# Kernel optimization log

Measured on AMD Instinct MI355X. Metric: run time of the kernel, lower is better.

## Reference

```python
import jax, jax.numpy as jnp
import numpy as np

EPS = 1e-12  # torch F.normalize eps

def _l2norm(t):
    # normalize over last axis (N), clamp norm like torch.nn.functional.normalize
    n = jnp.linalg.norm(t, axis=-1, keepdims=True)
    return t / jnp.maximum(n, EPS)

def setup_inputs() -> dict:
    key = jax.random.key(0)
    ks = jax.random.split(key, 4)
    B, N, D, H = 8, 4096, 768, 16
    x = jax.random.normal(ks[0], (B, N, D), dtype=jnp.float32)
    w_qkv = jax.random.normal(ks[1], (D, 3 * D), dtype=jnp.float32) * (D ** -0.5)
    temperature = jnp.ones((H, 1, 1), dtype=jnp.float32)
    w_proj = jax.random.normal(ks[2], (D, D), dtype=jnp.float32) * (D ** -0.5)
    b_proj = jnp.zeros((D,), dtype=jnp.float32)
    return {"x": x, "w_qkv": w_qkv, "temperature": temperature,
            "w_proj": w_proj, "b_proj": b_proj}

def reference(x, w_qkv, temperature, w_proj, b_proj):
    B, N, D = x.shape
    H = temperature.shape[0]
    C = D // H
    # qkv linear (no bias), split last dim as (3, H, C), move to (3, B, H, C, N)
    qkv = (x @ w_qkv).reshape(B, N, 3, H, C).transpose(2, 0, 3, 4, 1)
    q, k, v = qkv[0], qkv[1], qkv[2]            # each [B, H, C, N]
    q = _l2norm(q)
    k = _l2norm(k)
    # cross-covariance attention: small CxC matrix per head
    attn = jnp.einsum('bhcn,bhdn->bhcd', q, k) * temperature  # [B,H,C,C]
    attn = jax.nn.softmax(attn, axis=-1)
    out = jnp.einsum('bhcd,bhdn->bhcn', attn, v)  # [B,H,C,N]
    out = out.transpose(0, 3, 1, 2).reshape(B, N, D)  # B N (H C)
    return out @ w_proj + b_proj
```

## Files before the change

kernel.cpp:

```cpp
#include <hip/hip_runtime.h>
#include <stdint.h>

typedef __attribute__((ext_vector_type(4))) float          f32x4;
typedef __attribute__((ext_vector_type(8))) short          bf16x8;
typedef __attribute__((ext_vector_type(8))) unsigned short u16x8;
typedef __attribute__((ext_vector_type(4))) unsigned short u16x4;

static __device__ __forceinline__ unsigned short f2bf(float f){
  uint32_t u = __builtin_bit_cast(uint32_t, f);
  u += 0x7FFFu + ((u >> 16) & 1u);
  return (unsigned short)(u >> 16);
}
static __device__ __forceinline__ float bf2f(unsigned short h){
  uint32_t u = ((uint32_t)h) << 16;
  return __builtin_bit_cast(float, u);
}

__global__ void k_cvt(const float* __restrict__ in, unsigned short* __restrict__ out, long n){
  long i = ((long)blockIdx.x * blockDim.x + threadIdx.x) * 8;
  if (i >= n) return;
  const f32x4* p = (const f32x4*)(in + i);
  f32x4 a = p[0], b = p[1];
  u16x8 o;
  #pragma unroll
  for (int j = 0; j < 4; j++){ o[j] = f2bf(a[j]); o[4+j] = f2bf(b[j]); }
  *(u16x8*)(out + i) = o;
}

__global__ void k_cvtwv(const float* __restrict__ w, unsigned short* __restrict__ out){
  const long idx = ((long)blockIdx.x * blockDim.x + threadIdx.x) * 8;
  const int e = (int)(idx / 768), hd = (int)(idx - (long)e * 768);
  const float* s = w + (long)e * 2304 + 1536 + hd;
  f32x4 a = *(const f32x4*)s, b = *(const f32x4*)(s + 4);
  u16x8 o;
  #pragma unroll
  for (int j = 0; j < 4; j++){ o[j] = f2bf(a[j]); o[4+j] = f2bf(b[j]); }
  *(u16x8*)(out + idx) = o;
}

__global__ void k_tconv(const float* __restrict__ in, unsigned short* __restrict__ out, int R, int C){
  __shared__ float tl[64][65];
  const int c0 = blockIdx.x * 64, r0 = blockIdx.y * 64;
  const int t = threadIdx.x;
  {
    const int lr = t >> 2, lc = (t & 3) * 16;
    const f32x4* s = (const f32x4*)(in + (long)(r0 + lr) * C + c0 + lc);
    #pragma unroll
    for (int q = 0; q < 4; q++){
      f32x4 v = s[q];
      #pragma unroll
      for (int j = 0; j < 4; j++) tl[lr][lc + q*4 + j] = v[j];
    }
  }
  __syncthreads();
  {
    const int oc = t >> 2, orr = (t & 3) * 16;
    u16x8 o0, o1;
    #pragma unroll
    for (int i = 0; i < 8; i++){ o0[i] = f2bf(tl[orr + i][oc]); o1[i] = f2bf(tl[orr + 8 + i][oc]); }
    u16x8* dst = (u16x8*)(out + (long)(c0 + oc) * R + r0 + orr);
    dst[0] = o0; dst[1] = o1;
  }
}


static __device__ __forceinline__ void stageA(const unsigned short* __restrict__ G, int row0, int ke,
                                              char* slot, int t){
  const int r  = t >> 2;
  const int ko = (t & 3) ^ ((r ^ (r >> 2)) & 3);
  const char* src = (const char*)(G + (long)(row0 + r) * 768 + ke + ko * 8);
  char* dst = slot + (t & 0x1C0) * 16;
  __builtin_amdgcn_global_load_lds((const __attribute__((address_space(1))) unsigned int*)src,
                                   (__attribute__((address_space(3))) unsigned int*)dst, 16, 0, 0);
}
static __device__ __forceinline__ void stageB(const unsigned short* __restrict__ G, int row0, int ke,
                                              char* slot, int t){
  #pragma unroll
  for (int l = 0; l < 2; l++){
    const int r  = l*128 + (t >> 2);
    const int ko = (t & 3) ^ ((r ^ (r >> 2)) & 3);
    const char* src = (const char*)(G + (long)(row0 + r) * 768 + ke + ko * 8);
    char* dst = slot + l*8192 + (t & 0x1C0) * 16;
    __builtin_amdgcn_global_load_lds((const __attribute__((address_space(1))) unsigned int*)src,
                                     (__attribute__((address_space(3))) unsigned int*)dst, 16, 0, 0);
  }
}

static __device__ __forceinline__ bf16x8 ldfrag(const char* slot, int row, int ko){
  const int k2 = (ko ^ (row ^ (row >> 2))) & 3;
  return *(const bf16x8*)(slot + row*64 + k2*16);
}

#define VM3 asm volatile("s_waitcnt vmcnt(3)" ::: "memory")
#define VM0 asm volatile("s_waitcnt vmcnt(0)" ::: "memory")

#define PHASE1(CUR, STAGE_STMT, WAIT_STMT) do {                                \
    bf16x8 af[4], bq[4];                                                       \
    _Pragma("unroll")                                                          \
    for (int ni = 0; ni < 4; ni++)                                             \
      bq[ni] = ldfrag(sB[CUR], wn*64 + ni*16 + arow, ko);                      \
    _Pragma("unroll")                                                          \
    for (int mi = 0; mi < 4; mi++)                                             \
      af[mi] = ldfrag(sA[CUR], wm*64 + mi*16 + arow, ko);                      \
    __builtin_amdgcn_s_barrier();                                              \
    __builtin_amdgcn_s_setprio(1);                                             \
    _Pragma("unroll")                                                          \
    for (int mi = 0; mi < 4; mi++)                                             \
      _Pragma("unroll")                                                        \
      for (int ni = 0; ni < 4; ni++)                                           \
        acc[mi][ni] = __builtin_amdgcn_mfma_f32_16x16x32_bf16(                 \
            af[mi], bq[ni], acc[mi][ni], 0, 0, 0);                             \
    __builtin_amdgcn_s_setprio(0);                                             \
    STAGE_STMT;                                                                \
    WAIT_STMT;                                                                 \
    __builtin_amdgcn_s_barrier();                                              \
  } while(0)

template<int MODE>
__global__ __launch_bounds__(512, 4)
void k_gemm3(const unsigned short* __restrict__ A, const unsigned short* __restrict__ BT,
             unsigned short* __restrict__ QT, unsigned short* __restrict__ KT,
             float* __restrict__ OUTF, const float* __restrict__ bias,
             float* __restrict__ nrmp)
{
  __shared__ __attribute__((aligned(16))) char lds[73728];
  constexpr int NT = (MODE == 0) ? 6 : 3;
  constexpr int NWG = 256 * NT;
  const int o  = blockIdx.x;
  const int wg = (o & 7) * (NWG >> 3) + (o >> 3);
  const int jt = wg % NT, mt = wg / NT;
  const int m0 = mt * 128, j0 = jt * 256;
  const int t = threadIdx.x, lane = t & 63, w = t >> 6;
  const int wm = w >> 2, wn = w & 3;
  const int arow = lane & 15, ko = lane >> 4;
  const unsigned short* BTb = (MODE == 1) ? BT + ((long)(m0 >> 12)) * 768 * 768 : BT;

  char* const sA[3] = {lds,          lds + 8192,          lds + 16384};
  char* const sB[3] = {lds + 24576,  lds + 24576 + 16384, lds + 24576 + 32768};

  f32x4 acc[4][4] = {};

  stageA(A, m0, 0,  sA[0], t);  stageB(BTb, j0, 0,  sB[0], t);
  stageA(A, m0, 32, sA[1], t);  stageB(BTb, j0, 32, sB[1], t);
  VM3;
  __builtin_amdgcn_s_barrier();

  #pragma unroll 1
  for (int g = 0; g < 7; ++g){
    const int ke2 = g * 96;
    PHASE1(0, { stageA(A, m0, ke2+64,  sA[2], t); stageB(BTb, j0, ke2+64,  sB[2], t); }, VM3);
    PHASE1(1, { stageA(A, m0, ke2+96,  sA[0], t); stageB(BTb, j0, ke2+96,  sB[0], t); }, VM3);
    PHASE1(2, { stageA(A, m0, ke2+128, sA[1], t); stageB(BTb, j0, ke2+128, sB[1], t); }, VM3);
  }
  PHASE1(0, { stageA(A, m0, 736, sA[2], t); stageB(BTb, j0, 736, sB[2], t); }, VM3);
  PHASE1(1, { ; }, VM0);
  PHASE1(2, { ; }, ;);

  if (MODE == 0){
    const int b = m0 >> 12;
    const int nb = (m0 & 4095) + wm*64 + (lane >> 4)*4;
    #pragma unroll
    for (int mi = 0; mi < 4; mi++){
      #pragma unroll
      for (int ni = 0; ni < 4; ni++){
        const int jc = j0 + wn*64 + ni*16 + (lane & 15);
        const int s  = (jc >= 768);
        const int jl = jc - s * 768;
        const int h  = jl / 48;
        const int c  = jl - h * 48;
        unsigned short* dst = (s ? KT : QT) + (((long)(b*16 + h) * 48 + c) << 12) + nb + mi*16;
        u16x4 pk;
        #pragma unroll
        for (int r = 0; r < 4; r++) pk[r] = f2bf(acc[mi][ni][r]);
        *(u16x4*)dst = pk;
      }
    }
    const int chunk = ((m0 & 4095) >> 6) + wm;
    #pragma unroll
    for (int ni = 0; ni < 4; ni++){
      float ss = 0.f;
      #pragma unroll
      for (int mi = 0; mi < 4; mi++)
        #pragma unroll
        for (int r = 0; r < 4; r++) ss += acc[mi][ni][r] * acc[mi][ni][r];
      ss += __shfl_xor(ss, 16);
      ss += __shfl_xor(ss, 32);
      if (lane < 16){
        const int jc = j0 + wn*64 + ni*16 + lane;
        const int s  = (jc >= 768);
        const int jl = jc - s * 768;
        const int h  = jl / 48;
        const int c  = jl - h * 48;
        const int prow = s*6144 + (b*16 + h)*48 + c;
        nrmp[(long)prow*64 + chunk] = ss;
      }
    }
  } else {
    #pragma unroll
    for (int mi = 0; mi < 4; mi++){
      #pragma unroll
      for (int ni = 0; ni < 4; ni++){
        const int jc = j0 + wn*64 + ni*16 + (lane & 15);
        const float bv = bias[jc];
        const long mr = (long)m0 + wm*64 + mi*16 + (lane >> 4)*4;
        #pragma unroll
        for (int r = 0; r < 4; r++) OUTF[(mr + r) * 768 + jc] = acc[mi][ni][r] + bv;
      }
    }
  }
}

__global__ __launch_bounds__(256)
void k_attn_part(const unsigned short* __restrict__ QT, const unsigned short* __restrict__ KT,
                 float* __restrict__ Spart)
{
  __shared__ float Sl[4][2304];
  const int bh = blockIdx.x, ksp = blockIdx.y;
  const int t = threadIdx.x, lane = t & 63, w = t >> 6;
  const unsigned short* qb = QT + ((long)bh * 48 << 12);
  const unsigned short* kb = KT + ((long)bh * 48 << 12);
  const int n00 = ksp * 1024 + w * 256;
  f32x4 acc[3][3] = {};
  for (int kt = 0; kt < 256; kt += 32){
    bf16x8 af[3], bfr[3];
    #pragma unroll
    for (int ci = 0; ci < 3; ci++)
      af[ci]  = *(const bf16x8*)(qb + ((long)(ci*16 + (lane & 15)) << 12) + n00 + kt + (lane >> 4) * 8);
    #pragma unroll
    for (int di = 0; di < 3; di++)
      bfr[di] = *(const bf16x8*)(kb + ((long)(di*16 + (lane & 15)) << 12) + n00 + kt + (lane >> 4) * 8);
    #pragma unroll
    for (int ci = 0; ci < 3; ci++)
      #pragma unroll
      for (int di = 0; di < 3; di++)
        acc[ci][di] = __builtin_amdgcn_mfma_f32_16x16x32_bf16(af[ci], bfr[di], acc[ci][di], 0, 0, 0);
  }
  #pragma unroll
  for (int ci = 0; ci < 3; ci++)
    #pragma unroll
    for (int di = 0; di < 3; di++)
      #pragma unroll
      for (int r = 0; r < 4; r++)
        Sl[w][(ci*16 + (lane >> 4)*4 + r) * 48 + di*16 + (lane & 15)] = acc[ci][di][r];
  __syncthreads();
  float* outp = Spart + ((long)ksp * 128 + bh) * 2304;
  for (int idx = t; idx < 2304; idx += 256)
    outp[idx] = Sl[0][idx] + Sl[1][idx] + Sl[2][idx] + Sl[3][idx];
}

__global__ void k_softmax(const float* __restrict__ Spart, const float* __restrict__ nrmp,
                          const float* __restrict__ temp, unsigned short* __restrict__ attnT)
{
  __shared__ float invq[48], invk[48];
  const int bh = blockIdx.x, h = bh & 15;
  const int c = threadIdx.x;
  if (c < 48){
    float sq = 0.f, sk = 0.f;
    const float* pq = nrmp + (long)(bh*48 + c) * 64;
    const float* pk = nrmp + (long)(6144 + bh*48 + c) * 64;
    #pragma unroll
    for (int i = 0; i < 64; i++){ sq += pq[i]; sk += pk[i]; }
    invq[c] = 1.0f / fmaxf(sqrtf(sq), 1e-12f);
    invk[c] = 1.0f / fmaxf(sqrtf(sk), 1e-12f);
  }
  __syncthreads();
  if (c < 48){
    const float scq = invq[c] * temp[h];
    float row[48];
    #pragma unroll
    for (int d = 0; d < 48; d++){
      long base = ((long)bh * 48 + c) * 48 + d;
      float v = Spart[base] + Spart[base + 128L*2304] + Spart[base + 256L*2304] + Spart[base + 384L*2304];
      row[d] = v * scq * invk[d];
    }
    float mx = -1e30f;
    #pragma unroll
    for (int d = 0; d < 48; d++) mx = fmaxf(mx, row[d]);
    float s = 0.f;
    #pragma unroll
    for (int d = 0; d < 48; d++){ row[d] = expf(row[d] - mx); s += row[d]; }
    const float inv = 1.0f / s;
    unsigned short* ob = attnT + (long)bh * 48 * 64;
    #pragma unroll
    for (int d = 0; d < 48; d++) ob[d*64 + c] = f2bf(row[d] * inv);
    u16x8 z = {};
    *(u16x8*)(ob + c*64 + 48) = z;
    *(u16x8*)(ob + c*64 + 56) = z;
  }
}

__global__ __launch_bounds__(256)
void k_wmod2(const unsigned short* __restrict__ WpT, const unsigned short* __restrict__ attnT,
             unsigned short* __restrict__ WmodT)
{
  const int j0 = blockIdx.x * 256, h = blockIdx.y, b = blockIdx.z;
  const int t = threadIdx.x, lane = t & 63, w = t >> 6;
  const unsigned short* wp = WpT + h * 48;
  const unsigned short* ab = attnT + ((long)(b*16 + h)) * 48 * 64;
  f32x4 acc[4][3] = {};
  #pragma unroll
  for (int kt = 0; kt < 64; kt += 32){
    bf16x8 bfr[3];
    #pragma unroll
    for (int ni = 0; ni < 3; ni++)
      bfr[ni] = *(const bf16x8*)(ab + (ni*16 + (lane & 15))*64 + kt + (lane >> 4)*8);
    #pragma unroll
    for (int mi = 0; mi < 4; mi++){
      const int j = j0 + w*64 + mi*16 + (lane & 15);
      bf16x8 a = *(const bf16x8*)(wp + (long)j*768 + kt + (lane >> 4)*8);
      #pragma unroll
      for (int ni = 0; ni < 3; ni++)
        acc[mi][ni] = __builtin_amdgcn_mfma_f32_16x16x32_bf16(a, bfr[ni], acc[mi][ni], 0, 0, 0);
    }
  }
  #pragma unroll
  for (int mi = 0; mi < 4; mi++)
    #pragma unroll
    for (int ni = 0; ni < 3; ni++)
      #pragma unroll
      for (int r = 0; r < 4; r++){
        const int j = j0 + w*64 + mi*16 + (lane >> 4)*4 + r;
        const int d = ni*16 + (lane & 15);
        WmodT[(long)b*589824 + (long)j*768 + h*48 + d] = f2bf(acc[mi][ni][r]);
      }
}

__global__ __launch_bounds__(256)
void k_comb(const unsigned short* __restrict__ A, const unsigned short* __restrict__ BT,
            unsigned short* __restrict__ OUT)
{
  __shared__ unsigned short As[128 * 32];
  __shared__ unsigned short Bs[128 * 32];
  const int m0 = blockIdx.y * 128;
  const int j0 = blockIdx.x * 128;
  const int t = threadIdx.x;
  const int lane = t & 63;
  const int w = t >> 6, wm = w >> 1, wn = w & 1;

  f32x4 acc[4][4] = {};

  for (int kt = 0; kt < 768; kt += 32){
    if (kt) __syncthreads();
    #pragma unroll
    for (int i = 0; i < 2; i++){
      const char* ga = (const char*)A  + (long)(m0 + i*64 + (t >> 2)) * 1536 + kt*2 + (t & 3) * 16;
      const char* gb = (const char*)BT + (long)(j0 + i*64 + (t >> 2)) * 1536 + kt*2 + (t & 3) * 16;
      char* la = (char*)As + i*4096 + (t & 0xC0) * 16;
      char* lb = (char*)Bs + i*4096 + (t & 0xC0) * 16;
      __builtin_amdgcn_global_load_lds((const __attribute__((address_space(1))) unsigned int*)ga,
                                       (__attribute__((address_space(3))) unsigned int*)la, 16, 0, 0);
      __builtin_amdgcn_global_load_lds((const __attribute__((address_space(1))) unsigned int*)gb,
                                       (__attribute__((address_space(3))) unsigned int*)lb, 16, 0, 0);
    }
    __syncthreads();
    bf16x8 af[4], bfr[4];
    #pragma unroll
    for (int mi = 0; mi < 4; mi++)
      af[mi]  = *(const bf16x8*)&As[(wm*64 + mi*16 + (lane & 15)) * 32 + (lane >> 4) * 8];
    #pragma unroll
    for (int ni = 0; ni < 4; ni++)
      bfr[ni] = *(const bf16x8*)&Bs[(wn*64 + ni*16 + (lane & 15)) * 32 + (lane >> 4) * 8];
    #pragma unroll
    for (int mi = 0; mi < 4; mi++)
      #pragma unroll
      for (int ni = 0; ni < 4; ni++)
        acc[mi][ni] = __builtin_amdgcn_mfma_f32_16x16x32_bf16(af[mi], bfr[ni], acc[mi][ni], 0, 0, 0);
  }

  #pragma unroll
  for (int mi = 0; mi < 4; mi++)
    #pragma unroll
    for (int ni = 0; ni < 4; ni++){
      const int jc = j0 + wn*64 + ni*16 + (lane & 15);
      const long mr = (long)m0 + wm*64 + mi*16 + (lane >> 4) * 4;
      #pragma unroll
      for (int r = 0; r < 4; r++) OUT[(mr + r) * 768 + jc] = f2bf(acc[mi][ni][r]);
    }
}

extern "C" void kernel_launch(void* const* d_in, const int* in_sizes, int n_in,
                              void* d_out, int out_size, void* d_ws, size_t ws_size,
                              hipStream_t stream)
{
  (void)in_sizes; (void)n_in; (void)out_size; (void)ws_size;
  const float* x      = (const float*)d_in[0];
  const float* w_qkv  = (const float*)d_in[1];
  const float* temp   = (const float*)d_in[2];
  const float* w_proj = (const float*)d_in[3];
  const float* b_proj = (const float*)d_in[4];
  float* outF = (float*)d_out;

  char* ws = (char*)d_ws;
  size_t off = 0;
  auto alloc = [&](size_t bytes)->char*{ char* p = ws + off; off += (bytes + 255) & ~(size_t)255; return p; };

  unsigned short* x_bf  = (unsigned short*)alloc(50331648);
  unsigned short* WT    = (unsigned short*)alloc(3538944);
  unsigned short* WpT   = (unsigned short*)alloc(1179648);
  unsigned short* WvB   = (unsigned short*)alloc(1179648);
  unsigned short* QT    = (unsigned short*)alloc(100663296);
  unsigned short* KT    = QT + (long)6144 * 4096;
  float* nrmp           = (float*)alloc(12288L * 64 * 4);
  float* Spart          = (float*)alloc(4L * 128 * 2304 * 4);
  unsigned short* attnT = (unsigned short*)alloc(128L * 48 * 64 * 2);
  unsigned short* WmodT = (unsigned short*)alloc(9437184);
  unsigned short* WcombT= (unsigned short*)alloc(9437184);

  k_cvt<<<12288, 256, 0, stream>>>(x, x_bf, 25165824L);
  k_tconv<<<dim3(36, 12), 256, 0, stream>>>(w_qkv, WT, 768, 2304);
  k_tconv<<<dim3(12, 12), 256, 0, stream>>>(w_proj, WpT, 768, 768);
  k_cvtwv<<<288, 256, 0, stream>>>(w_qkv, WvB);
  k_gemm3<0><<<1536, 512, 0, stream>>>(x_bf, WT, QT, KT, nullptr, nullptr, nrmp);
  k_attn_part<<<dim3(128, 4), 256, 0, stream>>>(QT, KT, Spart);
  k_softmax<<<128, 64, 0, stream>>>(Spart, nrmp, temp, attnT);
  k_wmod2<<<dim3(3, 16, 8), 256, 0, stream>>>(WpT, attnT, WmodT);
  k_comb<<<dim3(6, 48), 256, 0, stream>>>(WmodT, WvB, WcombT);
  k_gemm3<1><<<768, 512, 0, stream>>>(x_bf, WcombT, nullptr, nullptr, outF, b_proj, nullptr);
}
```

Before: 253.2 us.

## Load GEMM B operand directly to registers, shrink LDS to A-only ring

The B-tile (weight) fragments are now loaded straight from global memory into registers per wave, one K-step ahead, instead of being staged through LDS. This shrinks LDS from 72KB to 24KB, which may raise occupancy, and removes the LDS write/read traffic for B. The A-fragment loads are split so MFMAs can start after only two A reads, and wait counts are adjusted for the new load mix. The trade-off is that each wave issues its own uncoalesced-strided global loads for B with no sharing across waves, which adds L2 traffic and exposes global latency.

```diff
diff --git a/kernel.cpp b/kernel.cpp
--- a/kernel.cpp
+++ b/kernel.cpp
@@ -73,57 +73,63 @@
   __builtin_amdgcn_global_load_lds((const __attribute__((address_space(1))) unsigned int*)src,
                                    (__attribute__((address_space(3))) unsigned int*)dst, 16, 0, 0);
 }
-static __device__ __forceinline__ void stageB(const unsigned short* __restrict__ G, int row0, int ke,
-                                              char* slot, int t){
-  #pragma unroll
-  for (int l = 0; l < 2; l++){
-    const int r  = l*128 + (t >> 2);
-    const int ko = (t & 3) ^ ((r ^ (r >> 2)) & 3);
-    const char* src = (const char*)(G + (long)(row0 + r) * 768 + ke + ko * 8);
-    char* dst = slot + l*8192 + (t & 0x1C0) * 16;
-    __builtin_amdgcn_global_load_lds((const __attribute__((address_space(1))) unsigned int*)src,
-                                     (__attribute__((address_space(3))) unsigned int*)dst, 16, 0, 0);
-  }
-}
 
 static __device__ __forceinline__ bf16x8 ldfrag(const char* slot, int row, int ko){
   const int k2 = (ko ^ (row ^ (row >> 2))) & 3;
   return *(const bf16x8*)(slot + row*64 + k2*16);
 }
 
-#define VM3 asm volatile("s_waitcnt vmcnt(3)" ::: "memory")
-#define VM0 asm volatile("s_waitcnt vmcnt(0)" ::: "memory")
-
-#define PHASE1(CUR, STAGE_STMT, WAIT_STMT) do {                                \
-    bf16x8 af[4], bq[4];                                                       \
-    _Pragma("unroll")                                                          \
-    for (int ni = 0; ni < 4; ni++)                                             \
-      bq[ni] = ldfrag(sB[CUR], wn*64 + ni*16 + arow, ko);                      \
-    _Pragma("unroll")                                                          \
-    for (int mi = 0; mi < 4; mi++)                                             \
-      af[mi] = ldfrag(sA[CUR], wm*64 + mi*16 + arow, ko);                      \
-    __builtin_amdgcn_s_barrier();                                              \
-    __builtin_amdgcn_s_setprio(1);                                             \
-    _Pragma("unroll")                                                          \
-    for (int mi = 0; mi < 4; mi++)                                             \
+#define MFMA_(a,b,c) __builtin_amdgcn_mfma_f32_16x16x32_bf16(a,b,c,0,0,0)
+
+#define LDB4(KE)                                                               \
+    bqv[0] = *(const bf16x8*)(bbase + (KE));                                   \
+    bqv[1] = *(const bf16x8*)(bbase + 12288 + (KE));                           \
+    bqv[2] = *(const bf16x8*)(bbase + 24576 + (KE));                           \
+    bqv[3] = *(const bf16x8*)(bbase + 36864 + (KE));
+
+#define POSTN(KE1, SLOT2, KE2)                                                 \
+    LDB4(KE1)                                                                  \
+    stageA(A, m0, (KE2), (SLOT2), t);                                          \
+    __builtin_amdgcn_sched_barrier(0);                                         \
+    asm volatile("s_waitcnt vmcnt(5)" ::: "memory");                           \
+    __builtin_amdgcn_s_barrier();
+
+#define POSTT                                                                  \
+    LDB4(736)                                                                  \
+    __builtin_amdgcn_sched_barrier(0);                                         \
+    asm volatile("s_waitcnt vmcnt(4)" ::: "memory");                           \
+    __builtin_amdgcn_s_barrier();
+
+#define PH(CUR, POST) do {                                                     \
+    {                                                                          \
+      bf16x8 a0 = ldfrag(sA[CUR], wm64 +  0 + arow, ko);                       \
+      bf16x8 a1 = ldfrag(sA[CUR], wm64 + 16 + arow, ko);                       \
+      __builtin_amdgcn_s_setprio(1);                                           \
       _Pragma("unroll")                                                        \
-      for (int ni = 0; ni < 4; ni++)                                           \
-        acc[mi][ni] = __builtin_amdgcn_mfma_f32_16x16x32_bf16(                 \
-            af[mi], bq[ni], acc[mi][ni], 0, 0, 0);                             \
-    __builtin_amdgcn_s_setprio(0);                                             \
-    STAGE_STMT;                                                                \
-    WAIT_STMT;                                                                 \
-    __builtin_amdgcn_s_barrier();                                              \
+      for (int ni = 0; ni < 4; ni++) acc[0][ni] = MFMA_(a0, bqv[ni], acc[0][ni]); \
+      _Pragma("unroll")                                                        \
+      for (int ni = 0; ni < 4; ni++) acc[1][ni] = MFMA_(a1, bqv[ni], acc[1][ni]); \
+    }                                                                          \
+    {                                                                          \
+      bf16x8 a2 = ldfrag(sA[CUR], wm64 + 32 + arow, ko);                       \
+      bf16x8 a3 = ldfrag(sA[CUR], wm64 + 48 + arow, ko);                       \
+      _Pragma("unroll")                                                        \
+      for (int ni = 0; ni < 4; ni++) acc[2][ni] = MFMA_(a2, bqv[ni], acc[2][ni]); \
+      _Pragma("unroll")                                                        \
+      for (int ni = 0; ni < 4; ni++) acc[3][ni] = MFMA_(a3, bqv[ni], acc[3][ni]); \
+      __builtin_amdgcn_s_setprio(0);                                           \
+    }                                                                          \
+    POST                                                                       \
   } while(0)
 
 template<int MODE>
 __global__ __launch_bounds__(512, 4)
-void k_gemm3(const unsigned short* __restrict__ A, const unsigned short* __restrict__ BT,
+void k_gemm4(const unsigned short* __restrict__ A, const unsigned short* __restrict__ BT,
              unsigned short* __restrict__ QT, unsigned short* __restrict__ KT,
              float* __restrict__ OUTF, const float* __restrict__ bias,
              float* __restrict__ nrmp)
 {
-  __shared__ __attribute__((aligned(16))) char lds[73728];
+  __shared__ __attribute__((aligned(16))) char lds[24576];
   constexpr int NT = (MODE == 0) ? 6 : 3;
   constexpr int NWG = 256 * NT;
   const int o  = blockIdx.x;
@@ -132,29 +138,33 @@
   const int m0 = mt * 128, j0 = jt * 256;
   const int t = threadIdx.x, lane = t & 63, w = t >> 6;
   const int wm = w >> 2, wn = w & 3;
+  const int wm64 = wm * 64;
   const int arow = lane & 15, ko = lane >> 4;
-  const unsigned short* BTb = (MODE == 1) ? BT + ((long)(m0 >> 12)) * 768 * 768 : BT;
-
-  char* const sA[3] = {lds,          lds + 8192,          lds + 16384};
-  char* const sB[3] = {lds + 24576,  lds + 24576 + 16384, lds + 24576 + 32768};
+  const unsigned short* BTb = (MODE == 1) ? BT + ((long)(m0 >> 12)) * 589824 : BT;
+  const unsigned short* bbase = BTb + (long)(j0 + wn*64 + arow) * 768 + ko * 8;
+
+  char* const sA[3] = {lds, lds + 8192, lds + 16384};
 
   f32x4 acc[4][4] = {};
-
-  stageA(A, m0, 0,  sA[0], t);  stageB(BTb, j0, 0,  sB[0], t);
-  stageA(A, m0, 32, sA[1], t);  stageB(BTb, j0, 32, sB[1], t);
-  VM3;
+  bf16x8 bqv[4];
+
+  stageA(A, m0, 0,  sA[0], t);
+  stageA(A, m0, 32, sA[1], t);
+  LDB4(0)
+  __builtin_amdgcn_sched_barrier(0);
+  asm volatile("s_waitcnt vmcnt(5)" ::: "memory");
   __builtin_amdgcn_s_barrier();
 
   #pragma unroll 1
   for (int g = 0; g < 7; ++g){
-    const int ke2 = g * 96;
-    PHASE1(0, { stageA(A, m0, ke2+64,  sA[2], t); stageB(BTb, j0, ke2+64,  sB[2], t); }, VM3);
-    PHASE1(1, { stageA(A, m0, ke2+96,  sA[0], t); stageB(BTb, j0, ke2+96,  sB[0], t); }, VM3);
-    PHASE1(2, { stageA(A, m0, ke2+128, sA[1], t); stageB(BTb, j0, ke2+128, sB[1], t); }, VM3);
-  }
-  PHASE1(0, { stageA(A, m0, 736, sA[2], t); stageB(BTb, j0, 736, sB[2], t); }, VM3);
-  PHASE1(1, { ; }, VM0);
-  PHASE1(2, { ; }, ;);
+    const int kb = g * 96;
+    PH(0, POSTN(kb + 32,  sA[2], kb + 64));
+    PH(1, POSTN(kb + 64,  sA[0], kb + 96));
+    PH(2, POSTN(kb + 96,  sA[1], kb + 128));
+  }
+  PH(0, POSTN(704, sA[2], 736));
+  PH(1, POSTT);
+  PH(2, {});
 
   if (MODE == 0){
     const int b = m0 >> 12;
@@ -410,10 +420,10 @@
   k_tconv<<<dim3(36, 12), 256, 0, stream>>>(w_qkv, WT, 768, 2304);
   k_tconv<<<dim3(12, 12), 256, 0, stream>>>(w_proj, WpT, 768, 768);
   k_cvtwv<<<288, 256, 0, stream>>>(w_qkv, WvB);
-  k_gemm3<0><<<1536, 512, 0, stream>>>(x_bf, WT, QT, KT, nullptr, nullptr, nrmp);
+  k_gemm4<0><<<1536, 512, 0, stream>>>(x_bf, WT, QT, KT, nullptr, nullptr, nrmp);
   k_attn_part<<<dim3(128, 4), 256, 0, stream>>>(QT, KT, Spart);
   k_softmax<<<128, 64, 0, stream>>>(Spart, nrmp, temp, attnT);
   k_wmod2<<<dim3(3, 16, 8), 256, 0, stream>>>(WpT, attnT, WmodT);
   k_comb<<<dim3(6, 48), 256, 0, stream>>>(WmodT, WvB, WcombT);
-  k_gemm3<1><<<768, 512, 0, stream>>>(x_bf, WcombT, nullptr, nullptr, outF, b_proj, nullptr);
-}
+  k_gemm4<1><<<768, 512, 0, stream>>>(x_bf, WcombT, nullptr, nullptr, outF, b_proj, nullptr);
+}
```

Measured after the change: 340.1 us. +34.3%, slower.

## Fuse QK^T cross-covariance into the QK projection GEMM epilogue

Applied to the files above, without the earlier changes.

Reorders the Q/K columns of the qkv weight so each 192-wide tile holds the Q and K channels of two heads. The QK GEMM then computes partial C×C q·k^T products from its 128-token tile in LDS, instead of writing 100MB of bf16 Q/K to global memory and reading it back in a separate kernel. Partial sums are spread over 32 token chunks, and softmax now reduces these larger partial buffers. The GEMM uses 384-thread blocks with a simpler LDS swizzle, and the extra epilogue MFMA work and partial-reduction traffic are the tradeoff.

```diff
diff --git a/kernel.cpp b/kernel.cpp
--- a/kernel.cpp
+++ b/kernel.cpp
@@ -63,22 +63,58 @@
   }
 }
 
-
-static __device__ __forceinline__ void stageA(const unsigned short* __restrict__ G, int row0, int ke,
-                                              char* slot, int t){
+static __device__ __forceinline__ int mapW(int j){
+  const int isK = (j >= 768);
+  const int jj = j - isK * 768;
+  const int h = jj / 48, c = jj - h * 48;
+  return (h >> 1) * 192 + (h & 1) * 96 + isK * 48 + c;
+}
+__global__ void k_tconvQK(const float* __restrict__ in, unsigned short* __restrict__ out){
+  __shared__ float tl[64][65];
+  const int c0 = blockIdx.x * 64, r0 = blockIdx.y * 64;
+  const int t = threadIdx.x;
+  {
+    const int lr = t >> 2, lc = (t & 3) * 16;
+    const f32x4* s = (const f32x4*)(in + (long)(r0 + lr) * 2304 + c0 + lc);
+    #pragma unroll
+    for (int q = 0; q < 4; q++){
+      f32x4 v = s[q];
+      #pragma unroll
+      for (int j = 0; j < 4; j++) tl[lr][lc + q*4 + j] = v[j];
+    }
+  }
+  __syncthreads();
+  {
+    const int oc = t >> 2, orr = (t & 3) * 16;
+    u16x8 o0, o1;
+    #pragma unroll
+    for (int i = 0; i < 8; i++){ o0[i] = f2bf(tl[orr + i][oc]); o1[i] = f2bf(tl[orr + 8 + i][oc]); }
+    u16x8* dst = (u16x8*)(out + (long)mapW(c0 + oc) * 768 + r0 + orr);
+    dst[0] = o0; dst[1] = o1;
+  }
+}
+
+
+static __device__ __forceinline__ bf16x8 ldfrag(const char* slot, int row, int ko){
+  const int k2 = (ko ^ (row >> 1)) & 3;
+  return *(const bf16x8*)(slot + row*64 + k2*16);
+}
+
+static __device__ __forceinline__ void stageA512(const unsigned short* __restrict__ G, int row0, int ke,
+                                                 char* slot, int t){
   const int r  = t >> 2;
-  const int ko = (t & 3) ^ ((r ^ (r >> 2)) & 3);
+  const int ko = (t & 3) ^ ((r >> 1) & 3);
   const char* src = (const char*)(G + (long)(row0 + r) * 768 + ke + ko * 8);
   char* dst = slot + (t & 0x1C0) * 16;
   __builtin_amdgcn_global_load_lds((const __attribute__((address_space(1))) unsigned int*)src,
                                    (__attribute__((address_space(3))) unsigned int*)dst, 16, 0, 0);
 }
-static __device__ __forceinline__ void stageB(const unsigned short* __restrict__ G, int row0, int ke,
-                                              char* slot, int t){
+static __device__ __forceinline__ void stageB512(const unsigned short* __restrict__ G, int row0, int ke,
+                                                 char* slot, int t){
   #pragma unroll
   for (int l = 0; l < 2; l++){
     const int r  = l*128 + (t >> 2);
-    const int ko = (t & 3) ^ ((r ^ (r >> 2)) & 3);
+    const int ko = (t & 3) ^ ((r >> 1) & 3);
     const char* src = (const char*)(G + (long)(row0 + r) * 768 + ke + ko * 8);
     char* dst = slot + l*8192 + (t & 0x1C0) * 16;
     __builtin_amdgcn_global_load_lds((const __attribute__((address_space(1))) unsigned int*)src,
@@ -86,13 +122,42 @@
   }
 }
 
-static __device__ __forceinline__ bf16x8 ldfrag(const char* slot, int row, int ko){
-  const int k2 = (ko ^ (row ^ (row >> 2))) & 3;
-  return *(const bf16x8*)(slot + row*64 + k2*16);
-}
-
+static __device__ __forceinline__ void stageA384(const unsigned short* __restrict__ G, int row0, int ke,
+                                                 char* slot, int t){
+  {
+    const int r  = t >> 2;
+    const int ko = (t & 3) ^ ((r >> 1) & 3);
+    const char* src = (const char*)(G + (long)(row0 + r) * 768 + ke + ko * 8);
+    char* dst = slot + (t & 0x1C0) * 16;
+    __builtin_amdgcn_global_load_lds((const __attribute__((address_space(1))) unsigned int*)src,
+                                     (__attribute__((address_space(3))) unsigned int*)dst, 16, 0, 0);
+  }
+  if (t < 128){
+    const int r  = 96 + (t >> 2);
+    const int ko = (t & 3) ^ ((r >> 1) & 3);
+    const char* src = (const char*)(G + (long)(row0 + r) * 768 + ke + ko * 8);
+    char* dst = slot + 6144 + (t & 0x1C0) * 16;
+    __builtin_amdgcn_global_load_lds((const __attribute__((address_space(1))) unsigned int*)src,
+                                     (__attribute__((address_space(3))) unsigned int*)dst, 16, 0, 0);
+  }
+}
+static __device__ __forceinline__ void stageB384(const unsigned short* __restrict__ G, int row0, int ke,
+                                                 char* slot, int t){
+  #pragma unroll
+  for (int l = 0; l < 2; l++){
+    const int r  = l*96 + (t >> 2);
+    const int ko = (t & 3) ^ ((r >> 1) & 3);
+    const char* src = (const char*)(G + (long)(row0 + r) * 768 + ke + ko * 8);
+    char* dst = slot + l*6144 + (t & 0x1C0) * 16;
+    __builtin_amdgcn_global_load_lds((const __attribute__((address_space(1))) unsigned int*)src,
+                                     (__attribute__((address_space(3))) unsigned int*)dst, 16, 0, 0);
+  }
+}
+
+#define VM0 asm volatile("s_waitcnt vmcnt(0)" ::: "memory")
 #define VM3 asm volatile("s_waitcnt vmcnt(3)" ::: "memory")
-#define VM0 asm volatile("s_waitcnt vmcnt(0)" ::: "memory")
+#define GATEQK { if (w < 2) asm volatile("s_waitcnt vmcnt(4)" ::: "memory");   \
+                 else       asm volatile("s_waitcnt vmcnt(3)" ::: "memory"); }
 
 #define PHASE1(CUR, STAGE_STMT, WAIT_STMT) do {                                \
     bf16x8 af[4], bq[4];                                                       \
@@ -101,7 +166,7 @@
       bq[ni] = ldfrag(sB[CUR], wn*64 + ni*16 + arow, ko);                      \
     _Pragma("unroll")                                                          \
     for (int mi = 0; mi < 4; mi++)                                             \
-      af[mi] = ldfrag(sA[CUR], wm*64 + mi*16 + arow, ko);                      \
+      af[mi] = ldfrag(sA[CUR], wm64 + mi*16 + arow, ko);                       \
     __builtin_amdgcn_s_barrier();                                              \
     __builtin_amdgcn_s_setprio(1);                                             \
     _Pragma("unroll")                                                          \
@@ -116,163 +181,187 @@
     __builtin_amdgcn_s_barrier();                                              \
   } while(0)
 
-template<int MODE>
+__global__ __launch_bounds__(384, 3)
+void k_gemmQK(const unsigned short* __restrict__ A, const unsigned short* __restrict__ BT,
+              float* __restrict__ Spart, float* __restrict__ nrmp)
+{
+  __shared__ __attribute__((aligned(16))) char lds[61440];
+  const int o  = blockIdx.x;
+  const int wg = (o & 7) * 256 + (o >> 3);
+  const int jt = wg & 7, mt = wg >> 3;
+  const int m0 = mt * 128, j0 = jt * 192;
+  const int t = threadIdx.x, lane = t & 63, w = t >> 6;
+  const int wm = w >> 2 & 1;
+  const int wmr = (w < 3) ? 0 : 1;
+  const int wn  = (w < 3) ? w : w - 3;
+  const int wm64 = wmr * 64;
+  const int arow = lane & 15, ko = lane >> 4;
+  (void)wm;
+
+  char* const sA[3] = {lds,          lds + 8192,          lds + 16384};
+  char* const sB[3] = {lds + 24576,  lds + 24576 + 12288, lds + 24576 + 24576};
+
+  f32x4 acc[4][4] = {};
+
+  stageA384(A, m0, 0,  sA[0], t);  stageB384(BT, j0, 0,  sB[0], t);
+  stageA384(A, m0, 32, sA[1], t);  stageB384(BT, j0, 32, sB[1], t);
+  GATEQK;
+  __builtin_amdgcn_s_barrier();
+
+  #pragma unroll 1
+  for (int g = 0; g < 7; ++g){
+    const int kb = g * 96;
+    PHASE1(0, { stageA384(A, m0, kb+64,  sA[2], t); stageB384(BT, j0, kb+64,  sB[2], t); }, GATEQK);
+    PHASE1(1, { stageA384(A, m0, kb+96,  sA[0], t); stageB384(BT, j0, kb+96,  sB[0], t); }, GATEQK);
+    PHASE1(2, { stageA384(A, m0, kb+128, sA[1], t); stageB384(BT, j0, kb+128, sB[1], t); }, GATEQK);
+  }
+  PHASE1(0, { stageA384(A, m0, 736, sA[2], t); stageB384(BT, j0, 736, sB[2], t); }, GATEQK);
+  PHASE1(1, { ; }, VM0);
+  PHASE1(2, { ; }, ;);
+
+  const int b = m0 >> 12;
+  const int chunk = ((m0 & 4095) >> 6) + wmr;
+  #pragma unroll
+  for (int ni = 0; ni < 4; ni++){
+    float ss = 0.f;
+    #pragma unroll
+    for (int mi = 0; mi < 4; mi++)
+      #pragma unroll
+      for (int r = 0; r < 4; r++) ss += acc[mi][ni][r] * acc[mi][ni][r];
+    ss += __shfl_xor(ss, 16);
+    ss += __shfl_xor(ss, 32);
+    if (lane < 16){
+      const int jr = wn*64 + ni*16 + lane;
+      const int hl = jr / 96, rem = jr - hl*96;
+      const int isK = (rem >= 48), c = rem - isK*48;
+      const int prow = isK*6144 + (b*16 + jt*2 + hl)*48 + c;
+      nrmp[(long)prow*64 + chunk] = ss;
+    }
+  }
+  __syncthreads();
+  #pragma unroll
+  for (int mi = 0; mi < 4; mi++){
+    #pragma unroll
+    for (int ni = 0; ni < 4; ni++){
+      const int j = wn*64 + ni*16 + (lane & 15);
+      const int n = wm64 + mi*16 + (lane >> 4)*4;
+      u16x4 pk;
+      #pragma unroll
+      for (int r = 0; r < 4; r++) pk[r] = f2bf(acc[mi][ni][r]);
+      *(u16x4*)(lds + (long)j*272 + n*2) = pk;
+    }
+  }
+  __syncthreads();
+  {
+    const int hl = (w < 3) ? 0 : 1;
+    const int ci = (w < 3) ? w : w - 3;
+    f32x4 accs[3] = {};
+    #pragma unroll
+    for (int kt = 0; kt < 128; kt += 32){
+      const bf16x8 aq = *(const bf16x8*)(lds + (long)(hl*96 + ci*16 + (lane & 15))*272
+                                             + (kt + (lane >> 4)*8)*2);
+      #pragma unroll
+      for (int di = 0; di < 3; di++){
+        const bf16x8 bk = *(const bf16x8*)(lds + (long)(hl*96 + 48 + di*16 + (lane & 15))*272
+                                               + (kt + (lane >> 4)*8)*2);
+        accs[di] = __builtin_amdgcn_mfma_f32_16x16x32_bf16(aq, bk, accs[di], 0, 0, 0);
+      }
+    }
+    const int ksp = (m0 & 4095) >> 7;
+    float* Sb = Spart + ((long)ksp*128 + b*16 + jt*2 + hl) * 2304;
+    #pragma unroll
+    for (int di = 0; di < 3; di++)
+      #pragma unroll
+      for (int r = 0; r < 4; r++){
+        const int c = ci*16 + (lane >> 4)*4 + r;
+        const int d = di*16 + (lane & 15);
+        Sb[c*48 + d] = accs[di][r];
+      }
+  }
+}
+
 __global__ __launch_bounds__(512, 4)
-void k_gemm3(const unsigned short* __restrict__ A, const unsigned short* __restrict__ BT,
-             unsigned short* __restrict__ QT, unsigned short* __restrict__ KT,
-             float* __restrict__ OUTF, const float* __restrict__ bias,
-             float* __restrict__ nrmp)
+void k_gemmP(const unsigned short* __restrict__ A, const unsigned short* __restrict__ BT,
+             float* __restrict__ OUTF, const float* __restrict__ bias)
 {
   __shared__ __attribute__((aligned(16))) char lds[73728];
-  constexpr int NT = (MODE == 0) ? 6 : 3;
-  constexpr int NWG = 256 * NT;
   const int o  = blockIdx.x;
-  const int wg = (o & 7) * (NWG >> 3) + (o >> 3);
-  const int jt = wg % NT, mt = wg / NT;
+  const int wg = (o & 7) * 96 + (o >> 3);
+  const int jt = wg % 3, mt = wg / 3;
   const int m0 = mt * 128, j0 = jt * 256;
   const int t = threadIdx.x, lane = t & 63, w = t >> 6;
   const int wm = w >> 2, wn = w & 3;
+  const int wm64 = wm * 64;
   const int arow = lane & 15, ko = lane >> 4;
-  const unsigned short* BTb = (MODE == 1) ? BT + ((long)(m0 >> 12)) * 768 * 768 : BT;
+  const unsigned short* BTb = BT + ((long)(m0 >> 12)) * 589824;
 
   char* const sA[3] = {lds,          lds + 8192,          lds + 16384};
   char* const sB[3] = {lds + 24576,  lds + 24576 + 16384, lds + 24576 + 32768};
 
   f32x4 acc[4][4] = {};
 
-  stageA(A, m0, 0,  sA[0], t);  stageB(BTb, j0, 0,  sB[0], t);
-  stageA(A, m0, 32, sA[1], t);  stageB(BTb, j0, 32, sB[1], t);
+  stageA512(A, m0, 0,  sA[0], t);  stageB512(BTb, j0, 0,  sB[0], t);
+  stageA512(A, m0, 32, sA[1], t);  stageB512(BTb, j0, 32, sB[1], t);
   VM3;
   __builtin_amdgcn_s_barrier();
 
   #pragma unroll 1
   for (int g = 0; g < 7; ++g){
-    const int ke2 = g * 96;
-    PHASE1(0, { stageA(A, m0, ke2+64,  sA[2], t); stageB(BTb, j0, ke2+64,  sB[2], t); }, VM3);
-    PHASE1(1, { stageA(A, m0, ke2+96,  sA[0], t); stageB(BTb, j0, ke2+96,  sB[0], t); }, VM3);
-    PHASE1(2, { stageA(A, m0, ke2+128, sA[1], t); stageB(BTb, j0, ke2+128, sB[1], t); }, VM3);
-  }
-  PHASE1(0, { stageA(A, m0, 736, sA[2], t); stageB(BTb, j0, 736, sB[2], t); }, VM3);
+    const int kb = g * 96;
+    PHASE1(0, { stageA512(A, m0, kb+64,  sA[2], t); stageB512(BTb, j0, kb+64,  sB[2], t); }, VM3);
+    PHASE1(1, { stageA512(A, m0, kb+96,  sA[0], t); stageB512(BTb, j0, kb+96,  sB[0], t); }, VM3);
+    PHASE1(2, { stageA512(A, m0, kb+128, sA[1], t); stageB512(BTb, j0, kb+128, sB[1], t); }, VM3);
+  }
+  PHASE1(0, { stageA512(A, m0, 736, sA[2], t); stageB512(BTb, j0, 736, sB[2], t); }, VM3);
   PHASE1(1, { ; }, VM0);
   PHASE1(2, { ; }, ;);
 
-  if (MODE == 0){
-    const int b = m0 >> 12;
-    const int nb = (m0 & 4095) + wm*64 + (lane >> 4)*4;
-    #pragma unroll
-    for (int mi = 0; mi < 4; mi++){
-      #pragma unroll
-      for (int ni = 0; ni < 4; ni++){
-        const int jc = j0 + wn*64 + ni*16 + (lane & 15);
-        const int s  = (jc >= 768);
-        const int jl = jc - s * 768;
-        const int h  = jl / 48;
-        const int c  = jl - h * 48;
-        unsigned short* dst = (s ? KT : QT) + (((long)(b*16 + h) * 48 + c) << 12) + nb + mi*16;
-        u16x4 pk;
-        #pragma unroll
-        for (int r = 0; r < 4; r++) pk[r] = f2bf(acc[mi][ni][r]);
-        *(u16x4*)dst = pk;
-      }
-    }
-    const int chunk = ((m0 & 4095) >> 6) + wm;
+  #pragma unroll
+  for (int mi = 0; mi < 4; mi++){
     #pragma unroll
     for (int ni = 0; ni < 4; ni++){
-      float ss = 0.f;
-      #pragma unroll
-      for (int mi = 0; mi < 4; mi++)
-        #pragma unroll
-        for (int r = 0; r < 4; r++) ss += acc[mi][ni][r] * acc[mi][ni][r];
-      ss += __shfl_xor(ss, 16);
-      ss += __shfl_xor(ss, 32);
-      if (lane < 16){
-        const int jc = j0 + wn*64 + ni*16 + lane;
-        const int s  = (jc >= 768);
-        const int jl = jc - s * 768;
-        const int h  = jl / 48;
-        const int c  = jl - h * 48;
-        const int prow = s*6144 + (b*16 + h)*48 + c;
-        nrmp[(long)prow*64 + chunk] = ss;
-      }
-    }
-  } else {
-    #pragma unroll
-    for (int mi = 0; mi < 4; mi++){
-      #pragma unroll
-      for (int ni = 0; ni < 4; ni++){
-        const int jc = j0 + wn*64 + ni*16 + (lane & 15);
-        const float bv = bias[jc];
-        const long mr = (long)m0 + wm*64 + mi*16 + (lane >> 4)*4;
-        #pragma unroll
-        for (int r = 0; r < 4; r++) OUTF[(mr + r) * 768 + jc] = acc[mi][ni][r] + bv;
-      }
-    }
-  }
-}
-
-__global__ __launch_bounds__(256)
-void k_attn_part(const unsigned short* __restrict__ QT, const unsigned short* __restrict__ KT,
-                 float* __restrict__ Spart)
-{
-  __shared__ float Sl[4][2304];
-  const int bh = blockIdx.x, ksp = blockIdx.y;
-  const int t = threadIdx.x, lane = t & 63, w = t >> 6;
-  const unsigned short* qb = QT + ((long)bh * 48 << 12);
-  const unsigned short* kb = KT + ((long)bh * 48 << 12);
-  const int n00 = ksp * 1024 + w * 256;
-  f32x4 acc[3][3] = {};
-  for (int kt = 0; kt < 256; kt += 32){
-    bf16x8 af[3], bfr[3];
-    #pragma unroll
-    for (int ci = 0; ci < 3; ci++)
-      af[ci]  = *(const bf16x8*)(qb + ((long)(ci*16 + (lane & 15)) << 12) + n00 + kt + (lane >> 4) * 8);
-    #pragma unroll
-    for (int di = 0; di < 3; di++)
-      bfr[di] = *(const bf16x8*)(kb + ((long)(di*16 + (lane & 15)) << 12) + n00 + kt + (lane >> 4) * 8);
-    #pragma unroll
-    for (int ci = 0; ci < 3; ci++)
-      #pragma unroll
-      for (int di = 0; di < 3; di++)
-        acc[ci][di] = __builtin_amdgcn_mfma_f32_16x16x32_bf16(af[ci], bfr[di], acc[ci][di], 0, 0, 0);
-  }
-  #pragma unroll
-  for (int ci = 0; ci < 3; ci++)
-    #pragma unroll
-    for (int di = 0; di < 3; di++)
-      #pragma unroll
-      for (int r = 0; r < 4; r++)
-        Sl[w][(ci*16 + (lane >> 4)*4 + r) * 48 + di*16 + (lane & 15)] = acc[ci][di][r];
-  __syncthreads();
-  float* outp = Spart + ((long)ksp * 128 + bh) * 2304;
-  for (int idx = t; idx < 2304; idx += 256)
-    outp[idx] = Sl[0][idx] + Sl[1][idx] + Sl[2][idx] + Sl[3][idx];
+      const int jc = j0 + wn*64 + ni*16 + (lane & 15);
+      const float bv = bias[jc];
+      const long mr = (long)m0 + wm64 + mi*16 + (lane >> 4)*4;
+      #pragma unroll
+      for (int r = 0; r < 4; r++) OUTF[(mr + r) * 768 + jc] = acc[mi][ni][r] + bv;
+    }
+  }
 }
 
 __global__ void k_softmax(const float* __restrict__ Spart, const float* __restrict__ nrmp,
                           const float* __restrict__ temp, unsigned short* __restrict__ attnT)
 {
+  __shared__ float Ss[2304];
   __shared__ float invq[48], invk[48];
   const int bh = blockIdx.x, h = bh & 15;
-  const int c = threadIdx.x;
-  if (c < 48){
+  const int t = threadIdx.x;
+  f32x4 a0[9];
+  #pragma unroll
+  for (int v = 0; v < 9; v++) a0[v] = f32x4{0.f,0.f,0.f,0.f};
+  for (int p = 0; p < 32; p++){
+    const f32x4* src = (const f32x4*)(Spart + ((long)p*128 + bh)*2304);
+    #pragma unroll
+    for (int v = 0; v < 9; v++) a0[v] += src[v*64 + t];
+  }
+  #pragma unroll
+  for (int v = 0; v < 9; v++) *(f32x4*)(Ss + (v*64 + t)*4) = a0[v];
+  if (t < 48){
     float sq = 0.f, sk = 0.f;
-    const float* pq = nrmp + (long)(bh*48 + c) * 64;
-    const float* pk = nrmp + (long)(6144 + bh*48 + c) * 64;
+    const float* pq = nrmp + (long)(bh*48 + t) * 64;
+    const float* pk = nrmp + (long)(6144 + bh*48 + t) * 64;
     #pragma unroll
     for (int i = 0; i < 64; i++){ sq += pq[i]; sk += pk[i]; }
-    invq[c] = 1.0f / fmaxf(sqrtf(sq), 1e-12f);
-    invk[c] = 1.0f / fmaxf(sqrtf(sk), 1e-12f);
+    invq[t] = 1.0f / fmaxf(sqrtf(sq), 1e-12f);
+    invk[t] = 1.0f / fmaxf(sqrtf(sk), 1e-12f);
   }
   __syncthreads();
-  if (c < 48){
+  if (t < 48){
+    const int c = t;
     const float scq = invq[c] * temp[h];
     float row[48];
     #pragma unroll
-    for (int d = 0; d < 48; d++){
-      long base = ((long)bh * 48 + c) * 48 + d;
-      float v = Spart[base] + Spart[base + 128L*2304] + Spart[base + 256L*2304] + Spart[base + 384L*2304];
-      row[d] = v * scq * invk[d];
-    }
+    for (int d = 0; d < 48; d++) row[d] = Ss[c*48 + d] * scq * invk[d];
     float mx = -1e30f;
     #pragma unroll
     for (int d = 0; d < 48; d++) mx = fmaxf(mx, row[d]);
@@ -395,25 +484,22 @@
   auto alloc = [&](size_t bytes)->char*{ char* p = ws + off; off += (bytes + 255) & ~(size_t)255; return p; };
 
   unsigned short* x_bf  = (unsigned short*)alloc(50331648);
-  unsigned short* WT    = (unsigned short*)alloc(3538944);
+  unsigned short* WTr   = (unsigned short*)alloc(2359296);
   unsigned short* WpT   = (unsigned short*)alloc(1179648);
   unsigned short* WvB   = (unsigned short*)alloc(1179648);
-  unsigned short* QT    = (unsigned short*)alloc(100663296);
-  unsigned short* KT    = QT + (long)6144 * 4096;
   float* nrmp           = (float*)alloc(12288L * 64 * 4);
-  float* Spart          = (float*)alloc(4L * 128 * 2304 * 4);
+  float* Spart          = (float*)alloc(32L * 128 * 2304 * 4);
   unsigned short* attnT = (unsigned short*)alloc(128L * 48 * 64 * 2);
   unsigned short* WmodT = (unsigned short*)alloc(9437184);
   unsigned short* WcombT= (unsigned short*)alloc(9437184);
 
   k_cvt<<<12288, 256, 0, stream>>>(x, x_bf, 25165824L);
-  k_tconv<<<dim3(36, 12), 256, 0, stream>>>(w_qkv, WT, 768, 2304);
+  k_tconvQK<<<dim3(24, 12), 256, 0, stream>>>(w_qkv, WTr);
   k_tconv<<<dim3(12, 12), 256, 0, stream>>>(w_proj, WpT, 768, 768);
   k_cvtwv<<<288, 256, 0, stream>>>(w_qkv, WvB);
-  k_gemm3<0><<<1536, 512, 0, stream>>>(x_bf, WT, QT, KT, nullptr, nullptr, nrmp);
-  k_attn_part<<<dim3(128, 4), 256, 0, stream>>>(QT, KT, Spart);
+  k_gemmQK<<<2048, 384, 0, stream>>>(x_bf, WTr, Spart, nrmp);
   k_softmax<<<128, 64, 0, stream>>>(Spart, nrmp, temp, attnT);
   k_wmod2<<<dim3(3, 16, 8), 256, 0, stream>>>(WpT, attnT, WmodT);
   k_comb<<<dim3(6, 48), 256, 0, stream>>>(WmodT, WvB, WcombT);
-  k_gemm3<1><<<768, 512, 0, stream>>>(x_bf, WcombT, nullptr, nullptr, outF, b_proj, nullptr);
-}
+  k_gemmP<<<768, 512, 0, stream>>>(x_bf, WcombT, outF, b_proj);
+}
```

New measurement: 245.5 us. 3.0% less time.
